# Kernel tuning notes

Measured on AMD Instinct MI355X. Metric: run time of the kernel, lower is better.

## Reference

```python
import jax, jax.numpy as jnp
import numpy as np

H, KVH, HD = 32, 8, 128          # query heads, kv heads, head_dim
HIDDEN = H * HD                   # 4096
TOTAL_KV = 3072                   # sum of (start_pos + seqlen) over the batch (static)
ROPE_THETA = 10000.0


def setup_inputs() -> dict:
    key = jax.random.key(0)
    ks = jax.random.split(key, 4)
    x = jax.random.normal(ks[0], (1024, HIDDEN), jnp.float32)
    wqkv = jax.random.normal(ks[1], (HIDDEN, HIDDEN + 2 * KVH * HD), jnp.float32) * 0.02
    wo = jax.random.normal(ks[2], (HIDDEN, HIDDEN), jnp.float32) * 0.02
    # paged cache: [num_layers=1, 2(k/v), cache_slots, kv_heads, head_dim], holds post-RoPE prefixes
    kv_cache = jax.random.normal(ks[3], (1, 2, 8192, KVH, HD), jnp.float32) * 0.02
    # 4 ragged requests: seqlens [512,256,128,128], cached prefixes [0,512,1024,512]
    seqstarts = jnp.array([0, 512, 768, 896, 1024], jnp.int32)
    start_pos = jnp.array([0, 512, 1024, 512], jnp.int32)
    kvstarts = jnp.array([0, 512, 1280, 2432, 3072], jnp.int32)  # cumsum of start_pos+seqlen
    cachestarts = jnp.array([0, 1024, 2560, 4096], jnp.int32)    # page base per request
    return dict(x=x, wqkv=wqkv, wo=wo, kv_cache=kv_cache, seqstarts=seqstarts,
                kvstarts=kvstarts, cachestarts=cachestarts, start_pos=start_pos)


def _rope(t, pos):
    # interleaved (GPT-J style) rotary over full head_dim; t: [T, nheads, HD], pos: [T]
    d2 = HD // 2
    inv_freq = 1.0 / (ROPE_THETA ** (jnp.arange(d2, dtype=jnp.float32) / d2))
    ang = pos.astype(jnp.float32)[:, None] * inv_freq      # [T, d2]
    cos = jnp.cos(ang)[:, None, :]
    sin = jnp.sin(ang)[:, None, :]
    x1, x2 = t[..., 0::2], t[..., 1::2]
    r1 = x1 * cos - x2 * sin
    r2 = x1 * sin + x2 * cos
    return jnp.stack([r1, r2], axis=-1).reshape(t.shape)


def _forward(x, wqkv, wo, kv_cache, seqstarts, kvstarts, cachestarts, start_pos):
    T = x.shape[0]
    # fused QKV projection
    xqkv = (x @ wqkv).reshape(T, H + 2 * KVH, HD)
    xq, xk, xv = jnp.split(xqkv, [H, H + KVH], axis=1)   # [T,32,HD],[T,8,HD],[T,8,HD]

    # per-token batch id and absolute position (ragged via seqstarts)
    tok = jnp.arange(T)
    bq = jnp.searchsorted(seqstarts, tok, side='right') - 1
    pos_q = tok - seqstarts[bq] + start_pos[bq]
    xq = _rope(xq, pos_q)
    xk = _rope(xk, pos_q)

    # assemble ragged KV stream: cached prefix (paged cache) + freshly projected tokens
    kvtok = jnp.arange(TOTAL_KV)
    bkv = jnp.searchsorted(kvstarts, kvtok, side='right') - 1
    pkv = kvtok - kvstarts[bkv]                              # absolute kv position
    is_new = pkv >= start_pos[bkv]
    new_idx = jnp.clip(seqstarts[bkv] + pkv - start_pos[bkv], 0, T - 1)
    cache_idx = cachestarts[bkv] + pkv                       # paged slot for prefix
    keys = jnp.where(is_new[:, None, None], xk[new_idx], kv_cache[0, 0][cache_idx])
    vals = jnp.where(is_new[:, None, None], xv[new_idx], kv_cache[0, 1][cache_idx])

    # GQA: repeat kv heads to match query heads
    rep = H // KVH
    keys = jnp.repeat(keys, rep, axis=1)                     # [TOTAL_KV, 32, HD]
    vals = jnp.repeat(vals, rep, axis=1)

    scale = 1.0 / jnp.sqrt(jnp.float32(HD))
    scores = jnp.einsum('qhd,khd->hqk', xq, keys) * scale    # [32, T, TOTAL_KV]
    # ragged causal mask: same request and kv position <= query position
    mask = (bq[:, None] == bkv[None, :]) & (pkv[None, :] <= pos_q[:, None])
    scores = jnp.where(mask[None], scores, jnp.float32(-1e30))
    probs = jax.nn.softmax(scores, axis=-1)
    attn = jnp.einsum('hqk,khd->qhd', probs, vals)           # [T, 32, HD]
    return attn.reshape(T, HIDDEN) @ wo


def reference(x, wqkv, wo, kv_cache, seqstarts, kvstarts, cachestarts, start_pos):
    return _forward(x, wqkv, wo, kv_cache, seqstarts, kvstarts, cachestarts, start_pos)
```

## Files before the change

kernel.cpp:

```cpp
#include <hip/hip_runtime.h>
#include <hip/hip_bf16.h>
#include <math.h>
#include <stdint.h>

typedef __bf16 bf16;
typedef __attribute__((ext_vector_type(4))) float floatx4;
typedef __attribute__((ext_vector_type(8))) bf16 bf16x8;
typedef __attribute__((ext_vector_type(4))) bf16 bf16x4;

#define LDS_ASYNC16(gptr, lptr)                                                \
  __builtin_amdgcn_global_load_lds(                                            \
      (const __attribute__((address_space(1))) void*)(gptr),                   \
      (__attribute__((address_space(3))) void*)(lptr), 16, 0, 0)

__global__ __launch_bounds__(256) void k_cvt(const float* __restrict__ in,
                                             bf16* __restrict__ out) {
  int i = (blockIdx.x * 256 + threadIdx.x) * 4;
  float4 v = *(const float4*)(in + i);
  bf16x4 o;
  o[0] = (bf16)v.x; o[1] = (bf16)v.y; o[2] = (bf16)v.z; o[3] = (bf16)v.w;
  *(bf16x4*)(out + i) = o;
}

__global__ __launch_bounds__(256) void k_merge(const float* __restrict__ a,
                                               const float* __restrict__ b,
                                               float* __restrict__ out) {
  int i = (blockIdx.x * 256 + threadIdx.x) * 4;
  float4 va = *(const float4*)(a + i);
  float4 vb = *(const float4*)(b + i);
  float4 o;
  o.x = va.x + vb.x; o.y = va.y + vb.y; o.z = va.z + vb.z; o.w = va.w + vb.w;
  *(float4*)(out + i) = o;
}

__global__ __launch_bounds__(256) void k_transpose_cvt(const float* __restrict__ in,
                                                       bf16* __restrict__ out,
                                                       int K, int N) {
  __shared__ float tile[64][65];
  int k0 = blockIdx.y * 64, n0 = blockIdx.x * 64;
  int tid = threadIdx.x;
  int cg = tid & 15, rr = tid >> 4;
#pragma unroll
  for (int p = 0; p < 4; ++p) {
    int r = rr + p * 16;
    float4 v = *(const float4*)(in + (size_t)(k0 + r) * N + n0 + cg * 4);
    tile[r][cg * 4 + 0] = v.x; tile[r][cg * 4 + 1] = v.y;
    tile[r][cg * 4 + 2] = v.z; tile[r][cg * 4 + 3] = v.w;
  }
  __syncthreads();
#pragma unroll
  for (int p = 0; p < 4; ++p) {
    int n = rr + p * 16;
    bf16x4 o;
    o[0] = (bf16)tile[cg * 4 + 0][n];
    o[1] = (bf16)tile[cg * 4 + 1][n];
    o[2] = (bf16)tile[cg * 4 + 2][n];
    o[3] = (bf16)tile[cg * 4 + 3][n];
    *(bf16x4*)(out + (size_t)(n0 + n) * K + k0 + cg * 4) = o;
  }
}

__global__ __launch_bounds__(256) void k_gemm_bt(const bf16* __restrict__ A,
                                                 const bf16* __restrict__ B,
                                                 float* __restrict__ C,
                                                 int M, int N, int K, int ksplit) {
  __shared__ bf16 As[128 * 32];
  __shared__ bf16 Bs[128 * 32];
  int tid = threadIdx.x;
  int w = tid >> 6, lane = tid & 63;
  int lq = lane >> 4, l16 = lane & 15;
  int bm = blockIdx.y * 128, bn = blockIdx.x * 128;
  int wm = (w >> 1) * 64, wn = (w & 1) * 64;
  int kc = K / ksplit;
  int koff = blockIdx.z * kc;
  C += (size_t)blockIdx.z * M * N;
  floatx4 acc[4][4] = {};
  const bf16* Ab = A + (size_t)bm * K;
  const bf16* Bb = B + (size_t)bn * K;
  int srow = (lane >> 2);
  int scol = (((lane & 3) ^ ((srow >> 1) & 3))) * 8;
  int sa = (l16 >> 1) & 3;

  for (int k0 = koff; k0 < koff + kc; k0 += 32) {
#pragma unroll
    for (int c = 0; c < 2; ++c) {
      int r = w * 32 + c * 16 + srow;
      LDS_ASYNC16(Ab + (size_t)r * K + k0 + scol, &As[(w * 32 + c * 16) * 32]);
      LDS_ASYNC16(Bb + (size_t)r * K + k0 + scol, &Bs[(w * 32 + c * 16) * 32]);
    }
    __syncthreads();
    bf16x8 af[4], bfr[4];
#pragma unroll
    for (int i = 0; i < 4; ++i)
      af[i] = *(const bf16x8*)&As[(wm + i * 16 + l16) * 32 + (lq ^ sa) * 8];
#pragma unroll
    for (int j = 0; j < 4; ++j)
      bfr[j] = *(const bf16x8*)&Bs[(wn + j * 16 + l16) * 32 + (lq ^ sa) * 8];
#pragma unroll
    for (int i = 0; i < 4; ++i)
#pragma unroll
      for (int j = 0; j < 4; ++j)
        acc[i][j] = __builtin_amdgcn_mfma_f32_16x16x32_bf16(af[i], bfr[j],
                                                            acc[i][j], 0, 0, 0);
    __syncthreads();
  }
#pragma unroll
  for (int i = 0; i < 4; ++i)
#pragma unroll
    for (int j = 0; j < 4; ++j) {
      int m = bm + wm + i * 16 + lq * 4;
      int n = bn + wn + j * 16 + l16;
      float* cp = C + (size_t)m * N + n;
#pragma unroll
      for (int r = 0; r < 4; ++r) cp[(size_t)r * N] = acc[i][j][r];
    }
}

__global__ __launch_bounds__(256) void k_rope(const float* __restrict__ xp0,
                                              const float* __restrict__ xp1,
                                              bf16* __restrict__ qb,
                                              bf16* __restrict__ kb,
                                              const int* __restrict__ seqstarts,
                                              const int* __restrict__ start_pos) {
  int t = blockIdx.x;
  int s = 0;
  for (int i = 1; i < 4; ++i) if (seqstarts[i] <= t) s = i;
  float pos = (float)(t - seqstarts[s] + start_pos[s]);
  for (int wk = threadIdx.x; wk < 40 * 64; wk += 256) {
    int hh = wk >> 6, j = wk & 63;
    size_t idx = ((size_t)t * 48 + hh) * 128 + 2 * j;
    float2 a0 = *(const float2*)(xp0 + idx);
    float2 a1 = *(const float2*)(xp1 + idx);
    float x1 = a0.x + a1.x;
    float x2 = a0.y + a1.y;
    float invf = exp2f(-(float)j * 0.20762050593045935f);
    float ang = pos * invf;
    float sv, cv;
    sincosf(ang, &sv, &cv);
    float r1 = x1 * cv - x2 * sv;
    float r2 = x1 * sv + x2 * cv;
    unsigned int u1 = (unsigned int)__builtin_bit_cast(unsigned short, (bf16)r1);
    unsigned int u2 = (unsigned int)__builtin_bit_cast(unsigned short, (bf16)r2);
    unsigned int pk = u1 | (u2 << 16);
    unsigned int* dst = (hh < 32)
        ? (unsigned int*)(qb + ((size_t)t * 32 + hh) * 128)
        : (unsigned int*)(kb + ((size_t)t * 8 + (hh - 32)) * 128);
    dst[j] = pk;
  }
}

__global__ __launch_bounds__(256) void k_assemble_k(
    const bf16* __restrict__ xk, const float* __restrict__ ck,
    bf16* __restrict__ kall,
    const int* __restrict__ seqstarts, const int* __restrict__ kvstarts,
    const int* __restrict__ cachestarts, const int* __restrict__ start_pos) {
  int p = blockIdx.x;
  int b = 0;
  for (int i = 1; i < 4; ++i) if (kvstarts[i] <= p) b = i;
  int pkv = p - kvstarts[b];
  int tid = threadIdx.x;
  int hk = tid >> 5, d4 = (tid & 31) * 4;
  bf16* dst = kall + ((size_t)hk * 3072 + p) * 128 + d4;
  if (pkv >= start_pos[b]) {
    int tn = seqstarts[b] + pkv - start_pos[b];
    *(bf16x4*)dst = *(const bf16x4*)(xk + ((size_t)tn * 8 + hk) * 128 + d4);
  } else {
    int ci = cachestarts[b] + pkv;
    float4 v = *(const float4*)(ck + ((size_t)ci * 8 + hk) * 128 + d4);
    bf16x4 o;
    o[0] = (bf16)v.x; o[1] = (bf16)v.y; o[2] = (bf16)v.z; o[3] = (bf16)v.w;
    *(bf16x4*)dst = o;
  }
}

__global__ __launch_bounds__(256) void k_assemble_vT(
    const float* __restrict__ xp0, const float* __restrict__ xp1,
    const float* __restrict__ cv, bf16* __restrict__ vT,
    const int* __restrict__ seqstarts, const int* __restrict__ kvstarts,
    const int* __restrict__ cachestarts, const int* __restrict__ start_pos) {
  __shared__ float tile[64][130];
  int hk = blockIdx.y, p0 = blockIdx.x * 64;
  int tid = threadIdx.x;
  {
    int r = tid >> 2;
    int p = p0 + r;
    int b = 0;
    for (int i = 1; i < 4; ++i) if (kvstarts[i] <= p) b = i;
    int pkv = p - kvstarts[b];
    int f0 = (tid & 3) * 32;
    if (pkv >= start_pos[b]) {
      int tn = seqstarts[b] + pkv - start_pos[b];
      size_t base = (size_t)tn * 6144 + (40 + hk) * 128;
#pragma unroll
      for (int i = 0; i < 8; ++i) {
        float4 v0 = *(const float4*)(xp0 + base + f0 + i * 4);
        float4 v1 = *(const float4*)(xp1 + base + f0 + i * 4);
        tile[r][f0 + i * 4 + 0] = v0.x + v1.x;
        tile[r][f0 + i * 4 + 1] = v0.y + v1.y;
        tile[r][f0 + i * 4 + 2] = v0.z + v1.z;
        tile[r][f0 + i * 4 + 3] = v0.w + v1.w;
      }
    } else {
      int ci = cachestarts[b] + pkv;
      const float* src = cv + ((size_t)ci * 8 + hk) * 128;
#pragma unroll
      for (int i = 0; i < 8; ++i) {
        float4 v = *(const float4*)(src + f0 + i * 4);
        tile[r][f0 + i * 4 + 0] = v.x; tile[r][f0 + i * 4 + 1] = v.y;
        tile[r][f0 + i * 4 + 2] = v.z; tile[r][f0 + i * 4 + 3] = v.w;
      }
    }
  }
  __syncthreads();
  int d = tid >> 1, hf = tid & 1;
  bf16* dst = vT + ((size_t)hk * 128 + d) * 3072 + p0 + hf * 32;
#pragma unroll
  for (int q = 0; q < 4; ++q) {
    bf16x8 o;
#pragma unroll
    for (int e = 0; e < 8; ++e) o[e] = (bf16)tile[hf * 32 + q * 8 + e][d];
    *(bf16x8*)(dst + q * 8) = o;
  }
}

__global__ __launch_bounds__(256, 4) void k_attn(
    const bf16* __restrict__ qb, const bf16* __restrict__ kall,
    const bf16* __restrict__ vT, bf16* __restrict__ aout,
    const int* __restrict__ seqstarts, const int* __restrict__ kvstarts,
    const int* __restrict__ start_pos) {
  __shared__ bf16 Ks[64 * 128];
  __shared__ bf16 Vs[128 * 64];
  __shared__ bf16 Ps[64 * 64];
  int qbi = blockIdx.x, h = blockIdx.y, hk = h >> 2;
  int t0 = qbi * 64;
  int s = 0;
  for (int i = 1; i < 4; ++i) if (seqstarts[i] <= t0) s = i;
  int posbase = t0 - seqstarts[s] + start_pos[s];
  int kv0 = kvstarts[s];
  int nkv = posbase + 64;
  int tid = threadIdx.x, w = tid >> 6, lane = tid & 63;
  int lq = lane >> 4, l16 = lane & 15;

  bf16x8 qa[4];
#pragma unroll
  for (int kk = 0; kk < 4; ++kk)
    qa[kk] = *(const bf16x8*)(qb + (((size_t)(t0 + w * 16 + l16) * 32 + h) * 128 +
                                    kk * 32 + lq * 8));

  int krow = lane >> 4;
  int kchunk = ((lane & 15) ^ krow) ;
  int vrow = lane >> 3;
  int vchunk = ((lane & 7) ^ (vrow & 7));
  int sw8 = l16 & 7;

  float m_r[4], l_r[4];
  floatx4 oacc[8] = {};
#pragma unroll
  for (int rg = 0; rg < 4; ++rg) { m_r[rg] = -3.0e38f; l_r[rg] = 0.f; }
  const float scale = 0.08838834764831845f;

  for (int p0 = 0; p0 < nkv; p0 += 64) {
#pragma unroll
    for (int c = 0; c < 4; ++c) {
      int base_r = w * 16 + c * 4;
      int r = base_r + krow;
      int gch = (lane & 15) ^ ((c * 4 + krow) & 15);
      LDS_ASYNC16(kall + (((size_t)hk * 3072 + kv0 + p0 + r) * 128 + gch * 8),
                  &Ks[base_r * 128]);
    }
#pragma unroll
    for (int c = 0; c < 4; ++c) {
      int base_d = w * 32 + c * 8;
      int d = base_d + vrow;
      LDS_ASYNC16(vT + (((size_t)hk * 128 + d) * 3072 + kv0 + p0 + vchunk * 8),
                  &Vs[base_d * 64]);
    }
    __syncthreads();

    floatx4 sacc[4] = {};
#pragma unroll
    for (int kk = 0; kk < 4; ++kk)
#pragma unroll
      for (int j = 0; j < 4; ++j) {
        bf16x8 kb = *(const bf16x8*)&Ks[(j * 16 + l16) * 128 +
                                        ((kk * 4 + lq) ^ l16) * 8];
        sacc[j] = __builtin_amdgcn_mfma_f32_16x16x32_bf16(qa[kk], kb, sacc[j], 0, 0, 0);
      }

#pragma unroll
    for (int rg = 0; rg < 4; ++rg) {
      int qpos = posbase + w * 16 + lq * 4 + rg;
      float sv[4];
      float rmax = -3.0e38f;
#pragma unroll
      for (int j = 0; j < 4; ++j) {
        int pkv = p0 + j * 16 + l16;
        sv[j] = (pkv <= qpos) ? sacc[j][rg] * scale : -3.0e38f;
        rmax = fmaxf(rmax, sv[j]);
      }
#pragma unroll
      for (int off = 1; off < 16; off <<= 1)
        rmax = fmaxf(rmax, __shfl_xor(rmax, off, 64));
      float mnew = fmaxf(m_r[rg], rmax);
      float alpha = __expf(m_r[rg] - mnew);
      m_r[rg] = mnew;
      int prow = w * 16 + lq * 4 + rg;
      int pswz = (lq * 4 + rg) & 7;
      float psum = 0.f;
#pragma unroll
      for (int j = 0; j < 4; ++j) {
        float pv = __expf(sv[j] - mnew);
        psum += pv;
        int chunk = (j * 2 + (l16 >> 3)) ^ pswz;
        Ps[prow * 64 + chunk * 8 + (l16 & 7)] = (bf16)pv;
      }
#pragma unroll
      for (int off = 1; off < 16; off <<= 1) psum += __shfl_xor(psum, off, 64);
      l_r[rg] = l_r[rg] * alpha + psum;
#pragma unroll
      for (int nt = 0; nt < 8; ++nt) oacc[nt][rg] *= alpha;
    }

#pragma unroll
    for (int kk = 0; kk < 2; ++kk) {
      bf16x8 pa = *(const bf16x8*)&Ps[(w * 16 + l16) * 64 +
                                      ((kk * 4 + lq) ^ sw8) * 8];
#pragma unroll
      for (int nt = 0; nt < 8; ++nt) {
        bf16x8 vb = *(const bf16x8*)&Vs[(nt * 16 + l16) * 64 +
                                        ((kk * 4 + lq) ^ sw8) * 8];
        oacc[nt] = __builtin_amdgcn_mfma_f32_16x16x32_bf16(pa, vb, oacc[nt], 0, 0, 0);
      }
    }
    __syncthreads();
  }

#pragma unroll
  for (int rg = 0; rg < 4; ++rg) {
    float inv = 1.0f / l_r[rg];
    int t = t0 + w * 16 + lq * 4 + rg;
#pragma unroll
    for (int nt = 0; nt < 8; ++nt)
      aout[(size_t)t * 4096 + h * 128 + nt * 16 + l16] =
          (bf16)(oacc[nt][rg] * inv);
  }
}

extern "C" void kernel_launch(void* const* d_in, const int* in_sizes, int n_in,
                              void* d_out, int out_size, void* d_ws, size_t ws_size,
                              hipStream_t stream) {
  const float* x = (const float*)d_in[0];
  const float* wqkv = (const float*)d_in[1];
  const float* wo = (const float*)d_in[2];
  const float* kv = (const float*)d_in[3];
  const int* seqstarts = (const int*)d_in[4];
  const int* kvstarts = (const int*)d_in[5];
  const int* cachestarts = (const int*)d_in[6];
  const int* start_pos = (const int*)d_in[7];
  float* out = (float*)d_out;

  char* base = (char*)d_ws;
  size_t off = 0;
  auto carve = [&](size_t bytes) {
    void* r = base + off;
    off += (bytes + 255) & ~(size_t)255;
    return r;
  };
  bf16* x_bf    = (bf16*)carve(1024ull * 4096 * 2);
  bf16* wqkvT   = (bf16*)carve(6144ull * 4096 * 2);
  bf16* woT     = (bf16*)carve(4096ull * 4096 * 2);
  float* xqkv   = (float*)carve(2ull * 1024 * 6144 * 4);
  bf16* q_bf    = (bf16*)carve(1024ull * 32 * 128 * 2);
  bf16* xk_bf   = (bf16*)carve(1024ull * 8 * 128 * 2);
  bf16* k_all   = (bf16*)carve(8ull * 3072 * 128 * 2);
  bf16* vT_all  = (bf16*)carve(8ull * 128 * 3072 * 2);
  bf16* attn_bf = (bf16*)carve(1024ull * 4096 * 2);
  float* outp = (float*)wqkvT;

  float* xqkv1 = xqkv + 1024ull * 6144;
  const float* cache_v = kv + 8192ull * 8 * 128;

  k_cvt<<<4096, 256, 0, stream>>>(x, x_bf);
  k_transpose_cvt<<<dim3(96, 64), 256, 0, stream>>>(wqkv, wqkvT, 4096, 6144);
  k_transpose_cvt<<<dim3(64, 64), 256, 0, stream>>>(wo, woT, 4096, 4096);
  k_gemm_bt<<<dim3(48, 8, 2), 256, 0, stream>>>(x_bf, wqkvT, xqkv, 1024, 6144,
                                                4096, 2);
  k_rope<<<1024, 256, 0, stream>>>(xqkv, xqkv1, q_bf, xk_bf, seqstarts, start_pos);
  k_assemble_k<<<3072, 256, 0, stream>>>(xk_bf, kv, k_all, seqstarts, kvstarts,
                                         cachestarts, start_pos);
  k_assemble_vT<<<dim3(48, 8), 256, 0, stream>>>(xqkv, xqkv1, cache_v, vT_all,
                                                 seqstarts, kvstarts, cachestarts,
                                                 start_pos);
  k_attn<<<dim3(16, 32), 256, 0, stream>>>(q_bf, k_all, vT_all, attn_bf,
                                           seqstarts, kvstarts, start_pos);
  k_gemm_bt<<<dim3(32, 8, 2), 256, 0, stream>>>(attn_bf, woT, outp, 1024, 4096,
                                                4096, 2);
  k_merge<<<4096, 256, 0, stream>>>(outp, outp + 1024ull * 4096, out);
}
```

Measured before the change: 517.2 us.

## Split attention KV range into segments with a separate merge kernel

Attention blocks now process at most 512 KV positions each, using a third grid dimension for segments. Each block writes unnormalized partial outputs plus row max and sum, and a new merge kernel rescales and combines them into the bf16 output. This aims to balance the uneven per-request KV lengths and raise parallelism. In exchange it adds fp32 partial-output traffic and an extra launch, and it reuses the QKV scratch buffer for the partials.

```diff
diff --git a/kernel.cpp b/kernel.cpp
--- a/kernel.cpp
+++ b/kernel.cpp
@@ -223,21 +223,25 @@
   }
 }
 
-__global__ __launch_bounds__(256, 4) void k_attn(
+__global__ __launch_bounds__(256) void k_attn(
     const bf16* __restrict__ qb, const bf16* __restrict__ kall,
-    const bf16* __restrict__ vT, bf16* __restrict__ aout,
+    const bf16* __restrict__ vT, float* __restrict__ pO,
+    float2* __restrict__ pml,
     const int* __restrict__ seqstarts, const int* __restrict__ kvstarts,
     const int* __restrict__ start_pos) {
   __shared__ bf16 Ks[64 * 128];
   __shared__ bf16 Vs[128 * 64];
   __shared__ bf16 Ps[64 * 64];
-  int qbi = blockIdx.x, h = blockIdx.y, hk = h >> 2;
+  int qbi = blockIdx.x, h = blockIdx.y, seg = blockIdx.z, hk = h >> 2;
   int t0 = qbi * 64;
   int s = 0;
   for (int i = 1; i < 4; ++i) if (seqstarts[i] <= t0) s = i;
   int posbase = t0 - seqstarts[s] + start_pos[s];
   int kv0 = kvstarts[s];
   int nkv = posbase + 64;
+  int pbeg = seg * 512;
+  if (pbeg >= nkv) return;
+  int pend = min(pbeg + 512, nkv);
   int tid = threadIdx.x, w = tid >> 6, lane = tid & 63;
   int lq = lane >> 4, l16 = lane & 15;
 
@@ -248,7 +252,6 @@
                                     kk * 32 + lq * 8));
 
   int krow = lane >> 4;
-  int kchunk = ((lane & 15) ^ krow) ;
   int vrow = lane >> 3;
   int vchunk = ((lane & 7) ^ (vrow & 7));
   int sw8 = l16 & 7;
@@ -259,7 +262,7 @@
   for (int rg = 0; rg < 4; ++rg) { m_r[rg] = -3.0e38f; l_r[rg] = 0.f; }
   const float scale = 0.08838834764831845f;
 
-  for (int p0 = 0; p0 < nkv; p0 += 64) {
+  for (int p0 = pbeg; p0 < pend; p0 += 64) {
 #pragma unroll
     for (int c = 0; c < 4; ++c) {
       int base_r = w * 16 + c * 4;
@@ -335,14 +338,62 @@
     __syncthreads();
   }
 
+  size_t obase = (((size_t)seg * 16 + qbi) * 32 + h) * 8192;
 #pragma unroll
   for (int rg = 0; rg < 4; ++rg) {
-    float inv = 1.0f / l_r[rg];
-    int t = t0 + w * 16 + lq * 4 + rg;
+    int row = w * 16 + lq * 4 + rg;
 #pragma unroll
     for (int nt = 0; nt < 8; ++nt)
-      aout[(size_t)t * 4096 + h * 128 + nt * 16 + l16] =
-          (bf16)(oacc[nt][rg] * inv);
+      pO[obase + (size_t)row * 128 + nt * 16 + l16] = oacc[nt][rg];
+    if (l16 == 0)
+      pml[(((size_t)seg * 16 + qbi) * 32 + h) * 64 + row] =
+          make_float2(m_r[rg], l_r[rg]);
+  }
+}
+
+__global__ __launch_bounds__(256) void k_attn_merge(
+    const float* __restrict__ pO, const float2* __restrict__ pml,
+    bf16* __restrict__ aout,
+    const int* __restrict__ seqstarts, const int* __restrict__ start_pos) {
+  int qbi = blockIdx.x, h = blockIdx.y;
+  int t0 = qbi * 64;
+  int s = 0;
+  for (int i = 1; i < 4; ++i) if (seqstarts[i] <= t0) s = i;
+  int nkv = t0 - seqstarts[s] + start_pos[s] + 64;
+  int ns = (nkv + 511) >> 9;
+  int tid = threadIdx.x;
+  int row = tid >> 2, cg = (tid & 3) * 32;
+  float2 ml[3];
+  float w[3];
+  float mstar = -3.0e38f;
+  for (int si = 0; si < ns; ++si) {
+    ml[si] = pml[(((size_t)si * 16 + qbi) * 32 + h) * 64 + row];
+    mstar = fmaxf(mstar, ml[si].x);
+  }
+  float denom = 0.f;
+  for (int si = 0; si < ns; ++si) {
+    w[si] = __expf(ml[si].x - mstar);
+    denom += w[si] * ml[si].y;
+  }
+  float inv = 1.0f / denom;
+  bf16* dst = aout + (size_t)(t0 + row) * 4096 + h * 128 + cg;
+#pragma unroll
+  for (int c = 0; c < 32; c += 8) {
+    float acc[8] = {};
+    for (int si = 0; si < ns; ++si) {
+      const float* src = pO + (((size_t)si * 16 + qbi) * 32 + h) * 8192 +
+                         (size_t)row * 128 + cg + c;
+      float4 v0 = *(const float4*)(src);
+      float4 v1 = *(const float4*)(src + 4);
+      acc[0] += w[si] * v0.x; acc[1] += w[si] * v0.y;
+      acc[2] += w[si] * v0.z; acc[3] += w[si] * v0.w;
+      acc[4] += w[si] * v1.x; acc[5] += w[si] * v1.y;
+      acc[6] += w[si] * v1.z; acc[7] += w[si] * v1.w;
+    }
+    bf16x8 o;
+#pragma unroll
+    for (int e = 0; e < 8; ++e) o[e] = (bf16)(acc[e] * inv);
+    *(bf16x8*)(dst + c) = o;
   }
 }
 
@@ -375,7 +426,9 @@
   bf16* k_all   = (bf16*)carve(8ull * 3072 * 128 * 2);
   bf16* vT_all  = (bf16*)carve(8ull * 128 * 3072 * 2);
   bf16* attn_bf = (bf16*)carve(1024ull * 4096 * 2);
+  float2* pml   = (float2*)carve(3ull * 16 * 32 * 64 * 8);
   float* outp = (float*)wqkvT;
+  float* pO = xqkv;
 
   float* xqkv1 = xqkv + 1024ull * 6144;
   const float* cache_v = kv + 8192ull * 8 * 128;
@@ -391,8 +444,10 @@
   k_assemble_vT<<<dim3(48, 8), 256, 0, stream>>>(xqkv, xqkv1, cache_v, vT_all,
                                                  seqstarts, kvstarts, cachestarts,
                                                  start_pos);
-  k_attn<<<dim3(16, 32), 256, 0, stream>>>(q_bf, k_all, vT_all, attn_bf,
-                                           seqstarts, kvstarts, start_pos);
+  k_attn<<<dim3(16, 32, 3), 256, 0, stream>>>(q_bf, k_all, vT_all, pO, pml,
+                                              seqstarts, kvstarts, start_pos);
+  k_attn_merge<<<dim3(16, 32), 256, 0, stream>>>(pO, pml, attn_bf, seqstarts,
+                                                 start_pos);
   k_gemm_bt<<<dim3(32, 8, 2), 256, 0, stream>>>(attn_bf, woT, outp, 1024, 4096,
                                                 4096, 2);
   k_merge<<<4096, 256, 0, stream>>>(outp, outp + 1024ull * 4096, out);
```

After: 498.0 us. -3.7%, faster.
